# Kernel tuning notes

Measured on AMD Instinct MI355X. Metric: run time of the kernel, lower is better.

## Reference

```python
import jax, jax.numpy as jnp
import numpy as np

# Daubechies-2 (db2) filter bank coefficients, as in pywt.Wavelet('db2')
_DEC_LO = np.array([-0.12940952255126037, 0.22414386804185735, 0.8365163037378079, 0.48296291314453416], dtype=np.float32)
_DEC_HI = np.array([-0.48296291314453416, 0.8365163037378079, -0.22414386804185735, -0.12940952255126037], dtype=np.float32)
_REC_LO = _DEC_LO[::-1].copy()
_REC_HI = _DEC_HI[::-1].copy()
_FLEN = 4


def _conv_valid(x, h):
    # np.convolve(x, h, 'valid') along last axis (true convolution: filter flipped)
    F = h.shape[0]
    N = x.shape[-1]
    hf = h[::-1]
    out = hf[0] * x[..., 0:N - F + 1]
    for k in range(1, F):
        out = out + hf[k] * x[..., k:N - F + 1 + k]
    return out


def dwt_db2(x):
    # pywt.dwt(x, 'db2') with default symmetric mode, axis=-1. x: (B, N) -> (B, (N+3)//2) x2
    xe = jnp.pad(x, ((0, 0), (_FLEN - 1, _FLEN - 1)), mode='symmetric')
    lo = jnp.asarray(_DEC_LO, dtype=x.dtype)
    hi = jnp.asarray(_DEC_HI, dtype=x.dtype)
    cA = _conv_valid(xe, lo)[..., 1::2]
    cD = _conv_valid(xe, hi)[..., 1::2]
    return cA, cD


def idwt_db2(cA, cD):
    # pywt.idwt(cA, cD, 'db2'): upsample-by-2 (len 2L-1), full conv with rec filters,
    # trim (flen-2) each side == pad by 1 and valid conv. Output length 2L - flen + 2.
    L = cA.shape[-1]
    def up(c):
        u = jnp.zeros(c.shape[:-1] + (2 * L - 1,), dtype=c.dtype)
        return u.at[..., ::2].set(c)
    uA = jnp.pad(up(cA), ((0, 0), (1, 1)))
    uD = jnp.pad(up(cD), ((0, 0), (1, 1)))
    rlo = jnp.asarray(_REC_LO, dtype=cA.dtype)
    rhi = jnp.asarray(_REC_HI, dtype=cA.dtype)
    return _conv_valid(uA, rlo) + _conv_valid(uD, rhi)


def setup_inputs() -> dict:
    key = jax.random.key(0)
    k1, k2 = jax.random.split(key)
    B, N = 4096, 4096
    output_dim = (N + 3) // 2  # 2049
    x = jax.random.normal(k1, (B, N), dtype=jnp.float32)
    # keras 'uniform' initializer: U(-0.05, 0.05), shape (input_shape[1], output_dim)
    kernel = jax.random.uniform(k2, (N, output_dim), dtype=jnp.float32, minval=-0.05, maxval=0.05)
    return {"x": x, "kernel": kernel}


def reference(x, kernel):
    cA, cD = dwt_db2(x)            # (B, L)
    cA = cA * kernel               # learned multiplicative gain
    cD = cD * kernel
    y = idwt_db2(cA, cD)           # (B, 2L - 2) == (B, N)
    return jax.nn.relu(y)
```

## Files before the change

### kernel.cpp

```cpp
#include <hip/hip_runtime.h>


#define BB 4096
#define NN 4096
#define LL 2049

__device__ __forceinline__ float xe_load(const float* s_x, int i ) {
    int idx = i - 3;
    idx = (idx < 0) ? (-idx - 1) : idx;
    idx = (idx >= NN) ? (2 * NN - 1 - idx) : idx;
    return s_x[idx];
}

__global__ __launch_bounds__(256) void wavelet_fused(const float* __restrict__ x,
                                                     const float* __restrict__ ker,
                                                     float* __restrict__ out) {
    __shared__ float s_x[NN];
    __shared__ float s_a[LL + 1];
    __shared__ float s_d[LL + 1];

    const int row = blockIdx.x;
    const int tid = threadIdx.x;

    const float lo0 = -0.12940952255126037f, lo1 = 0.22414386804185735f,
                lo2 =  0.8365163037378079f,  lo3 = 0.48296291314453416f;
    const float hi0 = -0.48296291314453416f, hi1 = 0.8365163037378079f,
                hi2 = -0.22414386804185735f, hi3 = -0.12940952255126037f;

    const float4* x4 = (const float4*)(x + (size_t)row * NN);
    float4* s_x4 = (float4*)s_x;
    #pragma unroll
    for (int i = tid; i < NN / 4; i += 256) s_x4[i] = x4[i];
    __syncthreads();

    const float* krow = ker + (size_t)row * LL;
    for (int j = tid; j < LL; j += 256) {
        const int m = 2 * j + 1;
        const float e0 = xe_load(s_x, m);
        const float e1 = xe_load(s_x, m + 1);
        const float e2 = xe_load(s_x, m + 2);
        const float e3 = xe_load(s_x, m + 3);
        const float cA = lo3 * e0 + lo2 * e1 + lo1 * e2 + lo0 * e3;
        const float cD = hi3 * e0 + hi2 * e1 + hi1 * e2 + hi0 * e3;
        const float g = krow[j];
        s_a[j] = cA * g;
        s_d[j] = cD * g;
    }
    __syncthreads();

    float2* out2 = (float2*)(out + (size_t)row * NN);
    for (int m = tid; m < NN / 2; m += 256) {
        const float a0 = s_a[m], a1 = s_a[m + 1];
        const float d0 = s_d[m], d1 = s_d[m + 1];
        float y0 = lo1 * a0 + lo3 * a1 + hi1 * d0 + hi3 * d1;
        float y1 = lo0 * a0 + lo2 * a1 + hi0 * d0 + hi2 * d1;
        y0 = fmaxf(y0, 0.0f);
        y1 = fmaxf(y1, 0.0f);
        out2[m] = make_float2(y0, y1);
    }
}

extern "C" void kernel_launch(void* const* d_in, const int* in_sizes, int n_in,
                              void* d_out, int out_size, void* d_ws, size_t ws_size,
                              hipStream_t stream) {
    const float* x   = (const float*)d_in[0];
    const float* ker = (const float*)d_in[1];
    float* out = (float*)d_out;
    wavelet_fused<<<dim3(BB), dim3(256), 0, stream>>>(x, ker, out);
}
```

Baseline: 152.1 us.

## Compute each output float4 in registers with halo loads instead of shared memory

Drops the shared-memory staging and the two block barriers. Each thread now loads its own float4 of x plus neighbouring float4s as a halo, recomputes three gained coefficient pairs (one of them redundantly with its neighbour) and writes one float4 of output. The grid becomes 4 blocks per row to give more parallelism and remove synchronisation. In exchange, neighbouring x loads and kernel loads are duplicated, though these should mostly hit in cache, and the unaligned kernel row loads stay scalar.

```diff
diff --git a/kernel.cpp b/kernel.cpp
--- a/kernel.cpp
+++ b/kernel.cpp
@@ -1,26 +1,15 @@
 #include <hip/hip_runtime.h>
 
 
-#define BB 4096
 #define NN 4096
 #define LL 2049
-
-__device__ __forceinline__ float xe_load(const float* s_x, int i ) {
-    int idx = i - 3;
-    idx = (idx < 0) ? (-idx - 1) : idx;
-    idx = (idx >= NN) ? (2 * NN - 1 - idx) : idx;
-    return s_x[idx];
-}
+#define PAIRS4 1024
 
 __global__ __launch_bounds__(256) void wavelet_fused(const float* __restrict__ x,
                                                      const float* __restrict__ ker,
                                                      float* __restrict__ out) {
-    __shared__ float s_x[NN];
-    __shared__ float s_a[LL + 1];
-    __shared__ float s_d[LL + 1];
-
-    const int row = blockIdx.x;
-    const int tid = threadIdx.x;
+    const int row = blockIdx.y;
+    const int t   = blockIdx.x * 256 + threadIdx.x;
 
     const float lo0 = -0.12940952255126037f, lo1 = 0.22414386804185735f,
                 lo2 =  0.8365163037378079f,  lo3 = 0.48296291314453416f;
@@ -28,36 +17,52 @@
                 hi2 = -0.22414386804185735f, hi3 = -0.12940952255126037f;
 
     const float4* x4 = (const float4*)(x + (size_t)row * NN);
-    float4* s_x4 = (float4*)s_x;
-    #pragma unroll
-    for (int i = tid; i < NN / 4; i += 256) s_x4[i] = x4[i];
-    __syncthreads();
+
+    const int tp = (t == 0) ? 0 : (t - 1);
+    const int tn = (t == PAIRS4 - 1) ? t : (t + 1);
+    const float4 vp = x4[tp];
+    const float4 vc = x4[t];
+    const float4 vn = x4[tn];
+
+    const bool first = (t == 0);
+    const bool last  = (t == PAIRS4 - 1);
+    const float e0 = first ? vc.y : vp.z;
+    const float e1 = first ? vc.x : vp.w;
+    const float e2 = vc.x;
+    const float e3 = vc.y;
+    const float e4 = vc.z;
+    const float e5 = vc.w;
+    const float e6 = last ? vc.w : vn.x;
+    const float e7 = last ? vc.z : vn.y;
 
     const float* krow = ker + (size_t)row * LL;
-    for (int j = tid; j < LL; j += 256) {
-        const int m = 2 * j + 1;
-        const float e0 = xe_load(s_x, m);
-        const float e1 = xe_load(s_x, m + 1);
-        const float e2 = xe_load(s_x, m + 2);
-        const float e3 = xe_load(s_x, m + 3);
-        const float cA = lo3 * e0 + lo2 * e1 + lo1 * e2 + lo0 * e3;
-        const float cD = hi3 * e0 + hi2 * e1 + hi1 * e2 + hi0 * e3;
-        const float g = krow[j];
-        s_a[j] = cA * g;
-        s_d[j] = cD * g;
-    }
-    __syncthreads();
+    const float g0 = krow[2 * t];
+    const float g1 = krow[2 * t + 1];
+    const float g2 = krow[2 * t + 2];
 
-    float2* out2 = (float2*)(out + (size_t)row * NN);
-    for (int m = tid; m < NN / 2; m += 256) {
-        const float a0 = s_a[m], a1 = s_a[m + 1];
-        const float d0 = s_d[m], d1 = s_d[m + 1];
-        float y0 = lo1 * a0 + lo3 * a1 + hi1 * d0 + hi3 * d1;
-        float y1 = lo0 * a0 + lo2 * a1 + hi0 * d0 + hi2 * d1;
-        y0 = fmaxf(y0, 0.0f);
-        y1 = fmaxf(y1, 0.0f);
-        out2[m] = make_float2(y0, y1);
-    }
+    const float cA0 = lo3 * e0 + lo2 * e1 + lo1 * e2 + lo0 * e3;
+    const float cD0 = hi3 * e0 + hi2 * e1 + hi1 * e2 + hi0 * e3;
+    const float cA1 = lo3 * e2 + lo2 * e3 + lo1 * e4 + lo0 * e5;
+    const float cD1 = hi3 * e2 + hi2 * e3 + hi1 * e4 + hi0 * e5;
+    const float cA2 = lo3 * e4 + lo2 * e5 + lo1 * e6 + lo0 * e7;
+    const float cD2 = hi3 * e4 + hi2 * e5 + hi1 * e6 + hi0 * e7;
+
+    const float A0 = g0 * cA0, D0 = g0 * cD0;
+    const float A1 = g1 * cA1, D1 = g1 * cD1;
+    const float A2 = g2 * cA2, D2 = g2 * cD2;
+
+    float y0 = lo1 * A0 + lo3 * A1 + hi1 * D0 + hi3 * D1;
+    float y1 = lo0 * A0 + lo2 * A1 + hi0 * D0 + hi2 * D1;
+    float y2 = lo1 * A1 + lo3 * A2 + hi1 * D1 + hi3 * D2;
+    float y3 = lo0 * A1 + lo2 * A2 + hi0 * D1 + hi2 * D2;
+
+    y0 = fmaxf(y0, 0.0f);
+    y1 = fmaxf(y1, 0.0f);
+    y2 = fmaxf(y2, 0.0f);
+    y3 = fmaxf(y3, 0.0f);
+
+    float4* out4 = (float4*)(out + (size_t)row * NN);
+    out4[t] = make_float4(y0, y1, y2, y3);
 }
 
 extern "C" void kernel_launch(void* const* d_in, const int* in_sizes, int n_in,
@@ -66,5 +71,5 @@
     const float* x   = (const float*)d_in[0];
     const float* ker = (const float*)d_in[1];
     float* out = (float*)d_out;
-    wavelet_fused<<<dim3(BB), dim3(256), 0, stream>>>(x, ker, out);
+    wavelet_fused<<<dim3(PAIRS4 / 256, 4096), dim3(256), 0, stream>>>(x, ker, out);
 }
```

Result: faster. 136.8 us (-10.1%).

## Compute wavelet per thread in registers with halo loads, removing shared memory

Applied to the files above, without the earlier changes.

Each thread now owns 8 consecutive outputs of a row. It loads its x slice plus a 2-element halo on each side (handling symmetric boundary reflection) and 5 kernel gains, then does the forward DWT, gain and inverse DWT entirely in registers. This removes shared-memory staging and both __syncthreads. The grid becomes 2 blocks per row, and outputs are written with nontemporal vector stores. Halo x values and one kernel gain are re-read by neighbouring threads, and the kernel-row loads are unaligned scalar reads.

```diff
diff --git a/kernel.cpp b/kernel.cpp
--- a/kernel.cpp
+++ b/kernel.cpp
@@ -1,63 +1,72 @@
 #include <hip/hip_runtime.h>
 
 
-#define BB 4096
 #define NN 4096
 #define LL 2049
+#define TPR 512
 
-__device__ __forceinline__ float xe_load(const float* s_x, int i ) {
-    int idx = i - 3;
-    idx = (idx < 0) ? (-idx - 1) : idx;
-    idx = (idx >= NN) ? (2 * NN - 1 - idx) : idx;
-    return s_x[idx];
-}
+typedef float v4f __attribute__((ext_vector_type(4)));
 
 __global__ __launch_bounds__(256) void wavelet_fused(const float* __restrict__ x,
                                                      const float* __restrict__ ker,
                                                      float* __restrict__ out) {
-    __shared__ float s_x[NN];
-    __shared__ float s_a[LL + 1];
-    __shared__ float s_d[LL + 1];
-
-    const int row = blockIdx.x;
-    const int tid = threadIdx.x;
+    const int row = blockIdx.y;
+    const int t   = blockIdx.x * 256 + threadIdx.x;
+    const int base = 8 * t;
 
     const float lo0 = -0.12940952255126037f, lo1 = 0.22414386804185735f,
                 lo2 =  0.8365163037378079f,  lo3 = 0.48296291314453416f;
     const float hi0 = -0.48296291314453416f, hi1 = 0.8365163037378079f,
                 hi2 = -0.22414386804185735f, hi3 = -0.12940952255126037f;
 
-    const float4* x4 = (const float4*)(x + (size_t)row * NN);
-    float4* s_x4 = (float4*)s_x;
+    const float* xrow = x + (size_t)row * NN;
+    const bool first = (t == 0);
+    const bool last  = (t == TPR - 1);
+
+    const float4 c0 = *(const float4*)(xrow + base);
+    const float4 c1 = *(const float4*)(xrow + base + 4);
+    const int la = first ? 0 : (base - 2);
+    const int ra = last ? (NN - 2) : (base + 8);
+    const float2 hl = *(const float2*)(xrow + la);
+    const float2 hr = *(const float2*)(xrow + ra);
+
+    float E[12];
+    E[0] = first ? hl.y : hl.x;
+    E[1] = first ? hl.x : hl.y;
+    E[2] = c0.x; E[3] = c0.y; E[4] = c0.z; E[5] = c0.w;
+    E[6] = c1.x; E[7] = c1.y; E[8] = c1.z; E[9] = c1.w;
+    E[10] = last ? hr.y : hr.x;
+    E[11] = last ? hr.x : hr.y;
+
+    const float* krow = ker + (size_t)row * LL + 4 * t;
+    float g[5];
     #pragma unroll
-    for (int i = tid; i < NN / 4; i += 256) s_x4[i] = x4[i];
-    __syncthreads();
+    for (int i = 0; i < 5; ++i) g[i] = krow[i];
 
-    const float* krow = ker + (size_t)row * LL;
-    for (int j = tid; j < LL; j += 256) {
-        const int m = 2 * j + 1;
-        const float e0 = xe_load(s_x, m);
-        const float e1 = xe_load(s_x, m + 1);
-        const float e2 = xe_load(s_x, m + 2);
-        const float e3 = xe_load(s_x, m + 3);
+    float A[5], D[5];
+    #pragma unroll
+    for (int i = 0; i < 5; ++i) {
+        const float e0 = E[2 * i], e1 = E[2 * i + 1], e2 = E[2 * i + 2], e3 = E[2 * i + 3];
         const float cA = lo3 * e0 + lo2 * e1 + lo1 * e2 + lo0 * e3;
         const float cD = hi3 * e0 + hi2 * e1 + hi1 * e2 + hi0 * e3;
-        const float g = krow[j];
-        s_a[j] = cA * g;
-        s_d[j] = cD * g;
+        A[i] = g[i] * cA;
+        D[i] = g[i] * cD;
     }
-    __syncthreads();
 
-    float2* out2 = (float2*)(out + (size_t)row * NN);
-    for (int m = tid; m < NN / 2; m += 256) {
-        const float a0 = s_a[m], a1 = s_a[m + 1];
-        const float d0 = s_d[m], d1 = s_d[m + 1];
-        float y0 = lo1 * a0 + lo3 * a1 + hi1 * d0 + hi3 * d1;
-        float y1 = lo0 * a0 + lo2 * a1 + hi0 * d0 + hi2 * d1;
-        y0 = fmaxf(y0, 0.0f);
-        y1 = fmaxf(y1, 0.0f);
-        out2[m] = make_float2(y0, y1);
+    float y[8];
+    #pragma unroll
+    for (int i = 0; i < 4; ++i) {
+        float ye = lo1 * A[i] + lo3 * A[i + 1] + hi1 * D[i] + hi3 * D[i + 1];
+        float yo = lo0 * A[i] + lo2 * A[i + 1] + hi0 * D[i] + hi2 * D[i + 1];
+        y[2 * i]     = fmaxf(ye, 0.0f);
+        y[2 * i + 1] = fmaxf(yo, 0.0f);
     }
+
+    float* orow = out + (size_t)row * NN + base;
+    v4f w0 = { y[0], y[1], y[2], y[3] };
+    v4f w1 = { y[4], y[5], y[6], y[7] };
+    __builtin_nontemporal_store(w0, (v4f*)orow);
+    __builtin_nontemporal_store(w1, (v4f*)(orow + 4));
 }
 
 extern "C" void kernel_launch(void* const* d_in, const int* in_sizes, int n_in,
@@ -66,5 +75,5 @@
     const float* x   = (const float*)d_in[0];
     const float* ker = (const float*)d_in[1];
     float* out = (float*)d_out;
-    wavelet_fused<<<dim3(BB), dim3(256), 0, stream>>>(x, ker, out);
+    wavelet_fused<<<dim3(TPR / 256, 4096), dim3(256), 0, stream>>>(x, ker, out);
 }
```

Measured after the change: 142.7 us. 1.07x faster.
